# Kernel tuning notes

Measured on AMD Instinct MI355X. Metric: run time of the kernel, lower is better.

## Reference

```python
import jax, jax.numpy as jnp
import numpy as np

N = 40000       # nodes
E = 512000      # edges (avg degree 16)
D = 128         # embed_dim
H = 128         # hidden_dim
R = 8           # num_relations
B = 8           # num_bases
C = 3           # output classes (hardcoded in conv7)


def _prelu(x, a):
    # torch.nn.PReLU(num_parameters=C): per-channel slope
    return jnp.where(x >= 0, x, a * x)


def _rgcn(x, src, dst, etype, bases, comp, root, bias):
    """PyG RGCNConv with basis decomposition, aggr='mean' (default).
    out[i] = sum_r mean_{e: dst=i, type=r} (W_r @ x[src_e]) + root @ x[i] + bias
    W_r = sum_b comp[r,b] * bases[b]. Aggregation is linear, so we aggregate
    source features per (node, relation) first, then apply W_r once per node.
    """
    n = x.shape[0]
    seg = dst * R + etype                      # composite (node, relation) id
    gx = x[src]                                # [E, in]  (big gather)
    agg = jax.ops.segment_sum(gx, seg, num_segments=n * R)              # [N*R, in]
    cnt = jax.ops.segment_sum(jnp.ones((src.shape[0],), x.dtype), seg,
                              num_segments=n * R)                        # [N*R]
    agg = agg / jnp.maximum(cnt, 1.0)[:, None]                           # mean per (node, rel)
    agg = agg.reshape(n, R, -1)                                          # [N, R, in]
    Wr = jnp.einsum('rb,bio->rio', comp, bases)                          # [R, in, out]
    return jnp.einsum('nri,rio->no', agg, Wr) + x @ root + bias


def setup_inputs() -> dict:
    key = jax.random.key(0)
    ks = jax.random.split(key, 20)
    num_x = jax.random.normal(ks[0], (N, 1), jnp.float32)
    x = jax.random.normal(ks[1], (N, D), jnp.float32)
    edge_index = jax.random.randint(ks[2], (2, E), 0, N, jnp.int32)
    edge_type = jax.random.randint(ks[3], (E,), 0, R, jnp.int32)
    # params
    lin_w = jax.random.normal(ks[4], (1, D), jnp.float32) * 0.1
    lin_b = jax.random.normal(ks[5], (D,), jnp.float32) * 0.1
    prelu_a = 0.25 + 0.01 * jax.random.normal(ks[6], (7, D), jnp.float32)
    s = 1.0 / np.sqrt(H)
    bases = jax.random.normal(ks[7], (6, B, H, H), jnp.float32) * s   # conv1..conv6 (in==out==H)
    comp = jax.random.normal(ks[8], (6, R, B), jnp.float32) * (1.0 / np.sqrt(B))
    root = jax.random.normal(ks[9], (6, H, H), jnp.float32) * s
    bias = jax.random.normal(ks[10], (6, H), jnp.float32) * 0.1
    bases7 = jax.random.normal(ks[11], (B, H, C), jnp.float32) * s
    comp7 = jax.random.normal(ks[12], (R, B), jnp.float32) * (1.0 / np.sqrt(B))
    root7 = jax.random.normal(ks[13], (H, C), jnp.float32) * s
    bias7 = jax.random.normal(ks[14], (C,), jnp.float32) * 0.1
    return dict(num_x=num_x, x=x, edge_index=edge_index, edge_type=edge_type,
                lin_w=lin_w, lin_b=lin_b, prelu_a=prelu_a,
                bases=bases, comp=comp, root=root, bias=bias,
                bases7=bases7, comp7=comp7, root7=root7, bias7=bias7)


def reference(num_x, x, edge_index, edge_type, lin_w, lin_b, prelu_a,
              bases, comp, root, bias, bases7, comp7, root7, bias7):
    src, dst = edge_index[0], edge_index[1]
    h = _prelu(num_x @ lin_w + lin_b, prelu_a[0])   # act_lin(num_lin(num_x))
    h = h + x
    for i in range(6):  # conv1..conv6 + PReLU (dropout is identity in eval)
        h = _rgcn(h, src, dst, edge_type, bases[i], comp[i], root[i], bias[i])
        h = _prelu(h, prelu_a[i + 1])
    h = _rgcn(h, src, dst, edge_type, bases7, comp7, root7, bias7)  # conv7 -> 3 classes
    return jax.nn.log_softmax(h, axis=1)
```

## Files before the change

kernel.cpp:

```cpp
#include <hip/hip_runtime.h>

typedef unsigned short ushortT;
typedef ushortT ushort8 __attribute__((ext_vector_type(8)));
typedef short bf16x8 __attribute__((ext_vector_type(8)));
typedef float f32x4 __attribute__((ext_vector_type(4)));
typedef unsigned int uint32;

#define NN 40000
#define NE 512000
#define DD 128
#define RR 8
#define NSEG (NN * RR)
#define KT 1152
#define NB_SCAN 1250

__device__ __forceinline__ float bf2f(ushortT u) { return __uint_as_float(((unsigned)u) << 16); }
__device__ __forceinline__ ushortT f2bf(float f) {
  unsigned u = __float_as_uint(f);
  unsigned r = (u + 0x7fffu + ((u >> 16) & 1u)) >> 16;
  return (ushortT)r;
}

__global__ void count_kernel(const int* __restrict__ dst, const int* __restrict__ et,
                             int* __restrict__ cnt) {
  int e = blockIdx.x * 256 + threadIdx.x;
  if (e < NE) atomicAdd(&cnt[dst[e] * RR + et[e]], 1);
}

__global__ void scan1_kernel(const int* __restrict__ cnt, int* __restrict__ offs,
                             int* __restrict__ bsum) {
  __shared__ int s[256];
  int tid = threadIdx.x, gid = blockIdx.x * 256 + tid;
  int v = cnt[gid];
  s[tid] = v; __syncthreads();
  for (int o = 1; o < 256; o <<= 1) {
    int t = (tid >= o) ? s[tid - o] : 0;
    __syncthreads(); s[tid] += t; __syncthreads();
  }
  offs[gid] = s[tid] - v;
  if (tid == 255) bsum[blockIdx.x] = s[255];
}

__global__ void scan2_kernel(int* __restrict__ bsum) {
  __shared__ int s[256];
  __shared__ int carry, tot;
  int tid = threadIdx.x;
  if (tid == 0) carry = 0;
  __syncthreads();
  for (int base = 0; base < NB_SCAN; base += 256) {
    int i = base + tid;
    int v = (i < NB_SCAN) ? bsum[i] : 0;
    s[tid] = v; __syncthreads();
    for (int o = 1; o < 256; o <<= 1) {
      int t = (tid >= o) ? s[tid - o] : 0;
      __syncthreads(); s[tid] += t; __syncthreads();
    }
    if (i < NB_SCAN) bsum[i] = s[tid] - v + carry;
    if (tid == 255) tot = s[255];
    __syncthreads();
    if (tid == 0) carry += tot;
    __syncthreads();
  }
}

__global__ void scan3_kernel(int* __restrict__ offs, const int* __restrict__ bsum,
                             const int* __restrict__ cnt, int* __restrict__ cursor) {
  int gid = blockIdx.x * 256 + threadIdx.x;
  int v = offs[gid] + bsum[blockIdx.x];
  offs[gid] = v;
  cursor[gid] = v;
  if (gid == NSEG - 1) offs[NSEG] = v + cnt[gid];
}

__global__ void fill_kernel(const int* __restrict__ src, const int* __restrict__ dst,
                            const int* __restrict__ et, int* __restrict__ cursor,
                            int* __restrict__ srcs) {
  int e = blockIdx.x * 256 + threadIdx.x;
  if (e >= NE) return;
  int seg = dst[e] * RR + et[e];
  int slot = atomicAdd(&cursor[seg], 1);
  srcs[slot] = src[e];
}

__global__ void init_h_kernel(const float* __restrict__ num_x, const float* __restrict__ x,
                              const float* __restrict__ lin_w, const float* __restrict__ lin_b,
                              const float* __restrict__ a0, ushortT* __restrict__ h) {
  int idx = blockIdx.x * 256 + threadIdx.x;
  if (idx >= NN * DD) return;
  int n = idx >> 7, d = idx & 127;
  float v = fmaf(num_x[n], lin_w[d], lin_b[d]);
  v = v >= 0.f ? v : a0[d] * v;
  h[idx] = f2bf(v + x[idx]);
}

__global__ void build_w_kernel(const float* __restrict__ bases, const float* __restrict__ comp,
                               const float* __restrict__ root, ushortT* __restrict__ Wt6) {
  int idx = blockIdx.x * 256 + threadIdx.x;
  if (idx >= 6 * DD * KT) return;
  int layer = idx / (DD * KT);
  int rem = idx - layer * (DD * KT);
  int j = rem / KT, k = rem - j * KT;
  const float* B  = bases + (size_t)layer * 8 * DD * DD;
  const float* C  = comp + layer * RR * 8;
  const float* Rt = root + (size_t)layer * DD * DD;
  float s;
  if (k < RR * DD) {
    int r = k >> 7, i = k & 127;
    s = 0.f;
#pragma unroll
    for (int b = 0; b < 8; ++b) s += C[r * 8 + b] * B[(b * DD + i) * DD + j];
  } else {
    s = Rt[(k - RR * DD) * DD + j];
  }
  Wt6[idx] = f2bf(s);
}

__global__ __launch_bounds__(256)
void agg_kernel(const int* __restrict__ offs, const int* __restrict__ srcs,
                const ushortT* __restrict__ h, ushortT* __restrict__ Xagg) {
  int seg = blockIdx.x * 32 + (threadIdx.x >> 3);
  int l = threadIdx.x & 7;
  int beg = offs[seg], end = offs[seg + 1];
  float a[16];
#pragma unroll
  for (int j = 0; j < 16; ++j) a[j] = 0.f;
  int e = beg;
  for (; e + 2 <= end; e += 2) {
    int s0 = srcs[e], s1 = srcs[e + 1];
    const ushortT* p0 = &h[(size_t)s0 * DD + l * 16];
    const ushortT* p1 = &h[(size_t)s1 * DD + l * 16];
    ushort8 v00 = *(const ushort8*)p0;
    ushort8 v01 = *(const ushort8*)(p0 + 8);
    ushort8 v10 = *(const ushort8*)p1;
    ushort8 v11 = *(const ushort8*)(p1 + 8);
#pragma unroll
    for (int j = 0; j < 8; ++j) {
      a[j]     += bf2f(v00[j]) + bf2f(v10[j]);
      a[8 + j] += bf2f(v01[j]) + bf2f(v11[j]);
    }
  }
  if (e < end) {
    int s0 = srcs[e];
    const ushortT* p0 = &h[(size_t)s0 * DD + l * 16];
    ushort8 v00 = *(const ushort8*)p0;
    ushort8 v01 = *(const ushort8*)(p0 + 8);
#pragma unroll
    for (int j = 0; j < 8; ++j) {
      a[j]     += bf2f(v00[j]);
      a[8 + j] += bf2f(v01[j]);
    }
  }
  float inv = (end > beg) ? 1.0f / (float)(end - beg) : 1.0f;
  ushort8 r0, r1;
#pragma unroll
  for (int j = 0; j < 8; ++j) {
    r0[j] = f2bf(a[j] * inv);
    r1[j] = f2bf(a[8 + j] * inv);
  }
  ushortT* op = &Xagg[(size_t)seg * DD + l * 16];
  *(ushort8*)op = r0;
  *(ushort8*)(op + 8) = r1;
}

__global__ __launch_bounds__(256)
void gemm_kernel(const ushortT* __restrict__ Xagg, const ushortT* __restrict__ h,
                 const ushortT* __restrict__ Wt, const float* __restrict__ bias,
                 const float* __restrict__ slope, ushortT* __restrict__ hout) {
  __shared__ ushortT As[64 * 64];
  __shared__ ushortT Bs[128 * 64];
  int tid = threadIdx.x, lane = tid & 63, wv = tid >> 6;
  int wr = wv >> 1, wc = wv & 1;
  int n0 = blockIdx.x * 64;
  int l8 = lane >> 3;
  int lp = lane & 7;
  f32x4 acc[2][4];
#pragma unroll
  for (int m = 0; m < 2; ++m)
#pragma unroll
    for (int n = 0; n < 4; ++n) acc[m][n] = (f32x4){0.f, 0.f, 0.f, 0.f};

  for (int kc = 0; kc < KT; kc += 64) {
#pragma unroll
    for (int j = 0; j < 2; ++j) {
      int row = wv * 16 + j * 8 + l8;
      int p = lp ^ (row & 7);
      const ushortT* g;
      if (kc < RR * DD) g = Xagg + (size_t)(n0 + row) * 1024 + kc + p * 8;
      else              g = h + (size_t)(n0 + row) * DD + (kc - RR * DD) + p * 8;
      __builtin_amdgcn_global_load_lds(
          (const __attribute__((address_space(1))) void*)g,
          (__attribute__((address_space(3))) void*)&As[(wv * 16 + j * 8) * 64], 16, 0, 0);
    }
#pragma unroll
    for (int j = 0; j < 4; ++j) {
      int col = wv * 32 + j * 8 + l8;
      int p = lp ^ (col & 7);
      const ushortT* g = Wt + (size_t)col * KT + kc + p * 8;
      __builtin_amdgcn_global_load_lds(
          (const __attribute__((address_space(1))) void*)g,
          (__attribute__((address_space(3))) void*)&Bs[(wv * 32 + j * 8) * 64], 16, 0, 0);
    }
    __syncthreads();
#pragma unroll
    for (int kk = 0; kk < 2; ++kk) {
      int ko2 = kk * 64 + (lane >> 4) * 16;
      bf16x8 a[2], b[4];
#pragma unroll
      for (int m = 0; m < 2; ++m) {
        int row = wr * 32 + m * 16 + (lane & 15);
        int off = ((row << 7) + ko2) ^ ((row & 7) << 4);
        a[m] = *(const bf16x8*)((const char*)As + off);
      }
#pragma unroll
      for (int n = 0; n < 4; ++n) {
        int col = wc * 64 + n * 16 + (lane & 15);
        int off = ((col << 7) + ko2) ^ ((col & 7) << 4);
        b[n] = *(const bf16x8*)((const char*)Bs + off);
      }
#pragma unroll
      for (int m = 0; m < 2; ++m)
#pragma unroll
        for (int n = 0; n < 4; ++n)
          acc[m][n] = __builtin_amdgcn_mfma_f32_16x16x32_bf16(a[m], b[n], acc[m][n], 0, 0, 0);
    }
    __syncthreads();
  }
#pragma unroll
  for (int m = 0; m < 2; ++m) {
    int row = n0 + wr * 32 + m * 16 + (lane >> 4) * 4;
#pragma unroll
    for (int n = 0; n < 4; ++n) {
      int col = wc * 64 + n * 16 + (lane & 15);
      float bcol = bias[col], scol = slope[col];
#pragma unroll
      for (int q = 0; q < 4; ++q) {
        float v = acc[m][n][q] + bcol;
        v = v >= 0.f ? v : scol * v;
        hout[(size_t)(row + q) * DD + col] = f2bf(v);
      }
    }
  }
}

__global__ void build_w7_kernel(const float* __restrict__ bases7, const float* __restrict__ comp7,
                                const float* __restrict__ root7, float* __restrict__ W7) {
  int idx = blockIdx.x * 256 + threadIdx.x;
  if (idx >= KT * 3) return;
  int row = idx / 3, c = idx - row * 3;
  if (row < RR * DD) {
    int r = row >> 7, i = row & 127;
    float s = 0.f;
#pragma unroll
    for (int b = 0; b < 8; ++b) s += comp7[r * 8 + b] * bases7[(b * DD + i) * 3 + c];
    W7[idx] = s;
  } else {
    W7[idx] = root7[(row - RR * DD) * 3 + c];
  }
}

__global__ void conv7_kernel(const ushortT* __restrict__ Xagg, const ushortT* __restrict__ h,
                             const float* __restrict__ W7, const float* __restrict__ bias7,
                             float* __restrict__ out) {
  int gw = (blockIdx.x * 256 + threadIdx.x) >> 6;
  if (gw >= NN) return;
  int lane = threadIdx.x & 63;
  float a0 = 0.f, a1 = 0.f, a2 = 0.f;
#pragma unroll
  for (int i = 0; i < 2; ++i) {
    int k0 = i * 512 + lane * 8;
    ushort8 v = *(const ushort8*)&Xagg[(size_t)gw * 1024 + k0];
#pragma unroll
    for (int j = 0; j < 8; ++j) {
      float xx = bf2f(v[j]);
      const float* w = &W7[(k0 + j) * 3];
      a0 = fmaf(xx, w[0], a0); a1 = fmaf(xx, w[1], a1); a2 = fmaf(xx, w[2], a2);
    }
  }
  {
    uint32 v = *(const uint32*)&h[(size_t)gw * DD + lane * 2];
    float x0 = __uint_as_float(v << 16), x1 = __uint_as_float(v & 0xffff0000u);
    int k0 = 1024 + lane * 2;
    const float* w0 = &W7[k0 * 3];
    const float* w1 = &W7[(k0 + 1) * 3];
    a0 = fmaf(x0, w0[0], a0); a1 = fmaf(x0, w0[1], a1); a2 = fmaf(x0, w0[2], a2);
    a0 = fmaf(x1, w1[0], a0); a1 = fmaf(x1, w1[1], a1); a2 = fmaf(x1, w1[2], a2);
  }
#pragma unroll
  for (int o = 32; o > 0; o >>= 1) {
    a0 += __shfl_down(a0, o);
    a1 += __shfl_down(a1, o);
    a2 += __shfl_down(a2, o);
  }
  if (lane == 0) {
    float l0 = a0 + bias7[0], l1 = a1 + bias7[1], l2 = a2 + bias7[2];
    float m = fmaxf(l0, fmaxf(l1, l2));
    float lse = m + logf(expf(l0 - m) + expf(l1 - m) + expf(l2 - m));
    out[gw * 3 + 0] = l0 - lse;
    out[gw * 3 + 1] = l1 - lse;
    out[gw * 3 + 2] = l2 - lse;
  }
}

extern "C" void kernel_launch(void* const* d_in, const int* in_sizes, int n_in,
                              void* d_out, int out_size, void* d_ws, size_t ws_size,
                              hipStream_t stream) {
  const float* num_x  = (const float*)d_in[0];
  const float* x      = (const float*)d_in[1];
  const int*   eidx   = (const int*)d_in[2];
  const int*   etype  = (const int*)d_in[3];
  const float* lin_w  = (const float*)d_in[4];
  const float* lin_b  = (const float*)d_in[5];
  const float* prelu  = (const float*)d_in[6];
  const float* bases  = (const float*)d_in[7];
  const float* comp   = (const float*)d_in[8];
  const float* root   = (const float*)d_in[9];
  const float* bias   = (const float*)d_in[10];
  const float* bases7 = (const float*)d_in[11];
  const float* comp7  = (const float*)d_in[12];
  const float* root7  = (const float*)d_in[13];
  const float* bias7  = (const float*)d_in[14];
  const int* srcv = eidx;
  const int* dstv = eidx + NE;
  float* out = (float*)d_out;

  char* p = (char*)d_ws;
  auto alloc = [&](size_t bytes) { char* q = p; p += (bytes + 255) & ~(size_t)255; return q; };
  int*     counts = (int*)alloc((size_t)NSEG * 4);
  int*     offs   = (int*)alloc((size_t)(NSEG + 1) * 4);
  int*     cursor = (int*)alloc((size_t)NSEG * 4);
  int*     bsum   = (int*)alloc((size_t)NB_SCAN * 4);
  int*     srcs   = (int*)alloc((size_t)NE * 4);
  ushortT* h0     = (ushortT*)alloc((size_t)NN * DD * 2);
  ushortT* h1     = (ushortT*)alloc((size_t)NN * DD * 2);
  ushortT* Xagg   = (ushortT*)alloc((size_t)NN * 1024 * 2);
  ushortT* Wt6    = (ushortT*)alloc((size_t)6 * DD * KT * 2);
  float*   W7     = (float*)alloc((size_t)KT * 3 * 4);
  if (ws_size < (size_t)(p - (char*)d_ws)) return;

  hipMemsetAsync(counts, 0, (size_t)NSEG * 4, stream);
  count_kernel<<<NE / 256, 256, 0, stream>>>(dstv, etype, counts);
  scan1_kernel<<<NB_SCAN, 256, 0, stream>>>(counts, offs, bsum);
  scan2_kernel<<<1, 256, 0, stream>>>(bsum);
  scan3_kernel<<<NB_SCAN, 256, 0, stream>>>(offs, bsum, counts, cursor);
  fill_kernel<<<NE / 256, 256, 0, stream>>>(srcv, dstv, etype, cursor, srcs);

  init_h_kernel<<<(NN * DD + 255) / 256, 256, 0, stream>>>(num_x, x, lin_w, lin_b, prelu, h0);
  build_w_kernel<<<(6 * DD * KT + 255) / 256, 256, 0, stream>>>(bases, comp, root, Wt6);
  build_w7_kernel<<<(KT * 3 + 255) / 256, 256, 0, stream>>>(bases7, comp7, root7, W7);

  ushortT* hin = h0;
  ushortT* hout = h1;
  for (int layer = 0; layer < 6; ++layer) {
    agg_kernel<<<NSEG / 32, 256, 0, stream>>>(offs, srcs, hin, Xagg);
    gemm_kernel<<<NN / 64, 256, 0, stream>>>(Xagg, hin, Wt6 + (size_t)layer * DD * KT,
                                             bias + layer * DD, prelu + (layer + 1) * DD, hout);
    ushortT* t = hin; hin = hout; hout = t;
  }
  agg_kernel<<<NSEG / 32, 256, 0, stream>>>(offs, srcs, hin, Xagg);
  conv7_kernel<<<NN / 4, 256, 0, stream>>>(Xagg, hin, W7, bias7, out);
}
```

Before: 474.9 us.

## Double-buffer GEMM LDS tiles and fuse conv7 projection into aggregation

The GEMM now keeps two LDS buffers and issues the next k-tile's global-to-LDS loads before computing the current one, so load latency can overlap the MFMA work. The final layer no longer writes the 80MB bf16 Xagg tensor and reads it back. Each (node, relation) segment is projected straight to the 3 output classes and accumulated with float atomics, and a small final kernel adds the root term and applies log_softmax. Costs are a larger LDS footprint per block, an extra memset, and atomic contention on 8 segments per node, whose float sums are not in a fixed order.

```diff
diff --git a/kernel.cpp b/kernel.cpp
--- a/kernel.cpp
+++ b/kernel.cpp
@@ -166,8 +166,8 @@
 void gemm_kernel(const ushortT* __restrict__ Xagg, const ushortT* __restrict__ h,
                  const ushortT* __restrict__ Wt, const float* __restrict__ bias,
                  const float* __restrict__ slope, ushortT* __restrict__ hout) {
-  __shared__ ushortT As[64 * 64];
-  __shared__ ushortT Bs[128 * 64];
+  __shared__ ushortT As[2][64 * 64];
+  __shared__ ushortT Bs[2][128 * 64];
   int tid = threadIdx.x, lane = tid & 63, wv = tid >> 6;
   int wr = wv >> 1, wc = wv & 1;
   int n0 = blockIdx.x * 64;
@@ -179,7 +179,8 @@
 #pragma unroll
     for (int n = 0; n < 4; ++n) acc[m][n] = (f32x4){0.f, 0.f, 0.f, 0.f};
 
-  for (int kc = 0; kc < KT; kc += 64) {
+  auto stage = [&](int buf, int t) {
+    int kc = t * 64;
 #pragma unroll
     for (int j = 0; j < 2; ++j) {
       int row = wv * 16 + j * 8 + l8;
@@ -189,7 +190,7 @@
       else              g = h + (size_t)(n0 + row) * DD + (kc - RR * DD) + p * 8;
       __builtin_amdgcn_global_load_lds(
           (const __attribute__((address_space(1))) void*)g,
-          (__attribute__((address_space(3))) void*)&As[(wv * 16 + j * 8) * 64], 16, 0, 0);
+          (__attribute__((address_space(3))) void*)&As[buf][(wv * 16 + j * 8) * 64], 16, 0, 0);
     }
 #pragma unroll
     for (int j = 0; j < 4; ++j) {
@@ -198,9 +199,15 @@
       const ushortT* g = Wt + (size_t)col * KT + kc + p * 8;
       __builtin_amdgcn_global_load_lds(
           (const __attribute__((address_space(1))) void*)g,
-          (__attribute__((address_space(3))) void*)&Bs[(wv * 32 + j * 8) * 64], 16, 0, 0);
-    }
-    __syncthreads();
+          (__attribute__((address_space(3))) void*)&Bs[buf][(wv * 32 + j * 8) * 64], 16, 0, 0);
+    }
+  };
+
+  stage(0, 0);
+  __syncthreads();
+  for (int t = 0; t < 18; ++t) {
+    int cur = t & 1;
+    if (t + 1 < 18) stage(cur ^ 1, t + 1);
 #pragma unroll
     for (int kk = 0; kk < 2; ++kk) {
       int ko2 = kk * 64 + (lane >> 4) * 16;
@@ -209,13 +216,13 @@
       for (int m = 0; m < 2; ++m) {
         int row = wr * 32 + m * 16 + (lane & 15);
         int off = ((row << 7) + ko2) ^ ((row & 7) << 4);
-        a[m] = *(const bf16x8*)((const char*)As + off);
+        a[m] = *(const bf16x8*)((const char*)As[cur] + off);
       }
 #pragma unroll
       for (int n = 0; n < 4; ++n) {
         int col = wc * 64 + n * 16 + (lane & 15);
         int off = ((col << 7) + ko2) ^ ((col & 7) << 4);
-        b[n] = *(const bf16x8*)((const char*)Bs + off);
+        b[n] = *(const bf16x8*)((const char*)Bs[cur] + off);
       }
 #pragma unroll
       for (int m = 0; m < 2; ++m)
@@ -258,33 +265,81 @@
   }
 }
 
-__global__ void conv7_kernel(const ushortT* __restrict__ Xagg, const ushortT* __restrict__ h,
-                             const float* __restrict__ W7, const float* __restrict__ bias7,
-                             float* __restrict__ out) {
+__global__ __launch_bounds__(256)
+void agg7c_kernel(const int* __restrict__ offs, const int* __restrict__ srcs,
+                  const ushortT* __restrict__ h, const float* __restrict__ W7,
+                  float* __restrict__ outacc) {
+  int seg = blockIdx.x * 32 + (threadIdx.x >> 3);
+  int l = threadIdx.x & 7;
+  int beg = offs[seg], end = offs[seg + 1];
+  if (end <= beg) return;
+  float a[16];
+#pragma unroll
+  for (int j = 0; j < 16; ++j) a[j] = 0.f;
+  int e = beg;
+  for (; e + 2 <= end; e += 2) {
+    int s0 = srcs[e], s1 = srcs[e + 1];
+    const ushortT* p0 = &h[(size_t)s0 * DD + l * 16];
+    const ushortT* p1 = &h[(size_t)s1 * DD + l * 16];
+    ushort8 v00 = *(const ushort8*)p0;
+    ushort8 v01 = *(const ushort8*)(p0 + 8);
+    ushort8 v10 = *(const ushort8*)p1;
+    ushort8 v11 = *(const ushort8*)(p1 + 8);
+#pragma unroll
+    for (int j = 0; j < 8; ++j) {
+      a[j]     += bf2f(v00[j]) + bf2f(v10[j]);
+      a[8 + j] += bf2f(v01[j]) + bf2f(v11[j]);
+    }
+  }
+  if (e < end) {
+    int s0 = srcs[e];
+    const ushortT* p0 = &h[(size_t)s0 * DD + l * 16];
+    ushort8 v00 = *(const ushort8*)p0;
+    ushort8 v01 = *(const ushort8*)(p0 + 8);
+#pragma unroll
+    for (int j = 0; j < 8; ++j) {
+      a[j]     += bf2f(v00[j]);
+      a[8 + j] += bf2f(v01[j]);
+    }
+  }
+  float inv = 1.0f / (float)(end - beg);
+  int r = seg & 7;
+  const float* w = &W7[((size_t)r * DD + l * 16) * 3];
+  float p0 = 0.f, p1 = 0.f, p2 = 0.f;
+#pragma unroll
+  for (int j = 0; j < 16; ++j) {
+    float x = a[j] * inv;
+    p0 = fmaf(x, w[j * 3 + 0], p0);
+    p1 = fmaf(x, w[j * 3 + 1], p1);
+    p2 = fmaf(x, w[j * 3 + 2], p2);
+  }
+#pragma unroll
+  for (int o = 1; o < 8; o <<= 1) {
+    p0 += __shfl_xor(p0, o);
+    p1 += __shfl_xor(p1, o);
+    p2 += __shfl_xor(p2, o);
+  }
+  if (l == 0) {
+    int node = seg >> 3;
+    atomicAdd(&outacc[node * 3 + 0], p0);
+    atomicAdd(&outacc[node * 3 + 1], p1);
+    atomicAdd(&outacc[node * 3 + 2], p2);
+  }
+}
+
+__global__ __launch_bounds__(256)
+void final_kernel(const float* __restrict__ outacc, const ushortT* __restrict__ h,
+                  const float* __restrict__ W7, const float* __restrict__ bias7,
+                  float* __restrict__ out) {
   int gw = (blockIdx.x * 256 + threadIdx.x) >> 6;
   if (gw >= NN) return;
   int lane = threadIdx.x & 63;
-  float a0 = 0.f, a1 = 0.f, a2 = 0.f;
-#pragma unroll
-  for (int i = 0; i < 2; ++i) {
-    int k0 = i * 512 + lane * 8;
-    ushort8 v = *(const ushort8*)&Xagg[(size_t)gw * 1024 + k0];
-#pragma unroll
-    for (int j = 0; j < 8; ++j) {
-      float xx = bf2f(v[j]);
-      const float* w = &W7[(k0 + j) * 3];
-      a0 = fmaf(xx, w[0], a0); a1 = fmaf(xx, w[1], a1); a2 = fmaf(xx, w[2], a2);
-    }
-  }
-  {
-    uint32 v = *(const uint32*)&h[(size_t)gw * DD + lane * 2];
-    float x0 = __uint_as_float(v << 16), x1 = __uint_as_float(v & 0xffff0000u);
-    int k0 = 1024 + lane * 2;
-    const float* w0 = &W7[k0 * 3];
-    const float* w1 = &W7[(k0 + 1) * 3];
-    a0 = fmaf(x0, w0[0], a0); a1 = fmaf(x0, w0[1], a1); a2 = fmaf(x0, w0[2], a2);
-    a0 = fmaf(x1, w1[0], a0); a1 = fmaf(x1, w1[1], a1); a2 = fmaf(x1, w1[2], a2);
-  }
+  uint32 v = *(const uint32*)&h[(size_t)gw * DD + lane * 2];
+  float x0 = __uint_as_float(v << 16), x1 = __uint_as_float(v & 0xffff0000u);
+  int k0 = (1024 + lane * 2) * 3;
+  float a0 = x0 * W7[k0 + 0] + x1 * W7[k0 + 3];
+  float a1 = x0 * W7[k0 + 1] + x1 * W7[k0 + 4];
+  float a2 = x0 * W7[k0 + 2] + x1 * W7[k0 + 5];
 #pragma unroll
   for (int o = 32; o > 0; o >>= 1) {
     a0 += __shfl_down(a0, o);
@@ -292,7 +347,9 @@
     a2 += __shfl_down(a2, o);
   }
   if (lane == 0) {
-    float l0 = a0 + bias7[0], l1 = a1 + bias7[1], l2 = a2 + bias7[2];
+    float l0 = a0 + outacc[gw * 3 + 0] + bias7[0];
+    float l1 = a1 + outacc[gw * 3 + 1] + bias7[1];
+    float l2 = a2 + outacc[gw * 3 + 2] + bias7[2];
     float m = fmaxf(l0, fmaxf(l1, l2));
     float lse = m + logf(expf(l0 - m) + expf(l1 - m) + expf(l2 - m));
     out[gw * 3 + 0] = l0 - lse;
@@ -335,9 +392,11 @@
   ushortT* Xagg   = (ushortT*)alloc((size_t)NN * 1024 * 2);
   ushortT* Wt6    = (ushortT*)alloc((size_t)6 * DD * KT * 2);
   float*   W7     = (float*)alloc((size_t)KT * 3 * 4);
+  float*   outacc = (float*)alloc((size_t)NN * 3 * 4);
   if (ws_size < (size_t)(p - (char*)d_ws)) return;
 
   hipMemsetAsync(counts, 0, (size_t)NSEG * 4, stream);
+  hipMemsetAsync(outacc, 0, (size_t)NN * 3 * 4, stream);
   count_kernel<<<NE / 256, 256, 0, stream>>>(dstv, etype, counts);
   scan1_kernel<<<NB_SCAN, 256, 0, stream>>>(counts, offs, bsum);
   scan2_kernel<<<1, 256, 0, stream>>>(bsum);
@@ -356,6 +415,6 @@
                                              bias + layer * DD, prelu + (layer + 1) * DD, hout);
     ushortT* t = hin; hin = hout; hout = t;
   }
-  agg_kernel<<<NSEG / 32, 256, 0, stream>>>(offs, srcs, hin, Xagg);
-  conv7_kernel<<<NN / 4, 256, 0, stream>>>(Xagg, hin, W7, bias7, out);
-}
+  agg7c_kernel<<<NSEG / 32, 256, 0, stream>>>(offs, srcs, hin, W7, outacc);
+  final_kernel<<<NN / 4, 256, 0, stream>>>(outacc, hin, W7, bias7, out);
+}
```

Result: slower. 495.3 us (+4.3%).

## Double-buffer GEMM LDS tiles and unroll edge gather by four

Applied to the files above, without the earlier changes.

The GEMM kernel now uses two LDS buffers for A and B. It issues the global-to-LDS loads for the next K chunk before running the MFMAs on the current chunk, so memory latency overlaps with compute. The aggregation kernel now processes four source edges per iteration, which keeps more gather loads in flight, and finishes the remainder with a scalar loop. In exchange, LDS use per block doubles, which may lower occupancy, and the agg kernel needs more registers.

```diff
diff --git a/kernel.cpp b/kernel.cpp
--- a/kernel.cpp
+++ b/kernel.cpp
@@ -125,25 +125,26 @@
 #pragma unroll
   for (int j = 0; j < 16; ++j) a[j] = 0.f;
   int e = beg;
-  for (; e + 2 <= end; e += 2) {
-    int s0 = srcs[e], s1 = srcs[e + 1];
+  for (; e + 4 <= end; e += 4) {
+    int s0 = srcs[e], s1 = srcs[e + 1], s2 = srcs[e + 2], s3 = srcs[e + 3];
     const ushortT* p0 = &h[(size_t)s0 * DD + l * 16];
     const ushortT* p1 = &h[(size_t)s1 * DD + l * 16];
-    ushort8 v00 = *(const ushort8*)p0;
-    ushort8 v01 = *(const ushort8*)(p0 + 8);
-    ushort8 v10 = *(const ushort8*)p1;
-    ushort8 v11 = *(const ushort8*)(p1 + 8);
+    const ushortT* p2 = &h[(size_t)s2 * DD + l * 16];
+    const ushortT* p3 = &h[(size_t)s3 * DD + l * 16];
+    ushort8 v00 = *(const ushort8*)p0, v01 = *(const ushort8*)(p0 + 8);
+    ushort8 v10 = *(const ushort8*)p1, v11 = *(const ushort8*)(p1 + 8);
+    ushort8 v20 = *(const ushort8*)p2, v21 = *(const ushort8*)(p2 + 8);
+    ushort8 v30 = *(const ushort8*)p3, v31 = *(const ushort8*)(p3 + 8);
 #pragma unroll
     for (int j = 0; j < 8; ++j) {
-      a[j]     += bf2f(v00[j]) + bf2f(v10[j]);
-      a[8 + j] += bf2f(v01[j]) + bf2f(v11[j]);
-    }
-  }
-  if (e < end) {
+      a[j]     += (bf2f(v00[j]) + bf2f(v10[j])) + (bf2f(v20[j]) + bf2f(v30[j]));
+      a[8 + j] += (bf2f(v01[j]) + bf2f(v11[j])) + (bf2f(v21[j]) + bf2f(v31[j]));
+    }
+  }
+  for (; e < end; ++e) {
     int s0 = srcs[e];
     const ushortT* p0 = &h[(size_t)s0 * DD + l * 16];
-    ushort8 v00 = *(const ushort8*)p0;
-    ushort8 v01 = *(const ushort8*)(p0 + 8);
+    ushort8 v00 = *(const ushort8*)p0, v01 = *(const ushort8*)(p0 + 8);
 #pragma unroll
     for (int j = 0; j < 8; ++j) {
       a[j]     += bf2f(v00[j]);
@@ -166,8 +167,8 @@
 void gemm_kernel(const ushortT* __restrict__ Xagg, const ushortT* __restrict__ h,
                  const ushortT* __restrict__ Wt, const float* __restrict__ bias,
                  const float* __restrict__ slope, ushortT* __restrict__ hout) {
-  __shared__ ushortT As[64 * 64];
-  __shared__ ushortT Bs[128 * 64];
+  __shared__ ushortT As[2][64 * 64];
+  __shared__ ushortT Bs[2][128 * 64];
   int tid = threadIdx.x, lane = tid & 63, wv = tid >> 6;
   int wr = wv >> 1, wc = wv & 1;
   int n0 = blockIdx.x * 64;
@@ -179,7 +180,8 @@
 #pragma unroll
     for (int n = 0; n < 4; ++n) acc[m][n] = (f32x4){0.f, 0.f, 0.f, 0.f};
 
-  for (int kc = 0; kc < KT; kc += 64) {
+  auto stage = [&](int buf, int t) {
+    int kc = t * 64;
 #pragma unroll
     for (int j = 0; j < 2; ++j) {
       int row = wv * 16 + j * 8 + l8;
@@ -189,7 +191,7 @@
       else              g = h + (size_t)(n0 + row) * DD + (kc - RR * DD) + p * 8;
       __builtin_amdgcn_global_load_lds(
           (const __attribute__((address_space(1))) void*)g,
-          (__attribute__((address_space(3))) void*)&As[(wv * 16 + j * 8) * 64], 16, 0, 0);
+          (__attribute__((address_space(3))) void*)&As[buf][(wv * 16 + j * 8) * 64], 16, 0, 0);
     }
 #pragma unroll
     for (int j = 0; j < 4; ++j) {
@@ -198,9 +200,15 @@
       const ushortT* g = Wt + (size_t)col * KT + kc + p * 8;
       __builtin_amdgcn_global_load_lds(
           (const __attribute__((address_space(1))) void*)g,
-          (__attribute__((address_space(3))) void*)&Bs[(wv * 32 + j * 8) * 64], 16, 0, 0);
-    }
-    __syncthreads();
+          (__attribute__((address_space(3))) void*)&Bs[buf][(wv * 32 + j * 8) * 64], 16, 0, 0);
+    }
+  };
+
+  stage(0, 0);
+  __syncthreads();
+  for (int t = 0; t < 18; ++t) {
+    int cur = t & 1;
+    if (t + 1 < 18) stage(cur ^ 1, t + 1);
 #pragma unroll
     for (int kk = 0; kk < 2; ++kk) {
       int ko2 = kk * 64 + (lane >> 4) * 16;
@@ -209,13 +217,13 @@
       for (int m = 0; m < 2; ++m) {
         int row = wr * 32 + m * 16 + (lane & 15);
         int off = ((row << 7) + ko2) ^ ((row & 7) << 4);
-        a[m] = *(const bf16x8*)((const char*)As + off);
+        a[m] = *(const bf16x8*)((const char*)As[cur] + off);
       }
 #pragma unroll
       for (int n = 0; n < 4; ++n) {
         int col = wc * 64 + n * 16 + (lane & 15);
         int off = ((col << 7) + ko2) ^ ((col & 7) << 4);
-        b[n] = *(const bf16x8*)((const char*)Bs + off);
+        b[n] = *(const bf16x8*)((const char*)Bs[cur] + off);
       }
 #pragma unroll
       for (int m = 0; m < 2; ++m)
```

Result: slower. 516.7 us (+8.8%).

## Double-buffer GEMM LDS tiles and stage edge source indices in shared memory

Applied to the files above, without the earlier changes.

The GEMM kernel now uses two LDS buffers, so it issues the async global-to-LDS loads for the next K tile while computing MFMAs on the current one, hiding load latency. The aggregation kernel cooperatively loads the block's segment offsets and up to ECAP source indices into shared memory before gathering, with a global fallback beyond the cap. The cost is doubled GEMM LDS usage, which may lower occupancy, and extra barriers in the aggregation kernel.

```diff
diff --git a/kernel.cpp b/kernel.cpp
--- a/kernel.cpp
+++ b/kernel.cpp
@@ -13,6 +13,7 @@
 #define NSEG (NN * RR)
 #define KT 1152
 #define NB_SCAN 1250
+#define ECAP 320
 
 __device__ __forceinline__ float bf2f(ushortT u) { return __uint_as_float(((unsigned)u) << 16); }
 __device__ __forceinline__ ushortT f2bf(float f) {
@@ -118,15 +119,28 @@
 __global__ __launch_bounds__(256)
 void agg_kernel(const int* __restrict__ offs, const int* __restrict__ srcs,
                 const ushortT* __restrict__ h, ushortT* __restrict__ Xagg) {
-  int seg = blockIdx.x * 32 + (threadIdx.x >> 3);
-  int l = threadIdx.x & 7;
-  int beg = offs[seg], end = offs[seg + 1];
+  __shared__ int s_offs[33];
+  __shared__ int s_srcs[ECAP];
+  int tid = threadIdx.x;
+  int sb = blockIdx.x * 32;
+  if (tid < 33) s_offs[tid] = offs[sb + tid];
+  __syncthreads();
+  int e_base = s_offs[0];
+  int nE = s_offs[32] - e_base;
+  for (int i = tid; i < nE && i < ECAP; i += 256) s_srcs[i] = srcs[e_base + i];
+  __syncthreads();
+
+  int g = tid >> 3;
+  int l = tid & 7;
+  int beg = s_offs[g], end = s_offs[g + 1];
   float a[16];
 #pragma unroll
   for (int j = 0; j < 16; ++j) a[j] = 0.f;
   int e = beg;
   for (; e + 2 <= end; e += 2) {
-    int s0 = srcs[e], s1 = srcs[e + 1];
+    int i0 = e - e_base, i1 = i0 + 1;
+    int s0 = (i0 < ECAP) ? s_srcs[i0] : srcs[e];
+    int s1 = (i1 < ECAP) ? s_srcs[i1] : srcs[e + 1];
     const ushortT* p0 = &h[(size_t)s0 * DD + l * 16];
     const ushortT* p1 = &h[(size_t)s1 * DD + l * 16];
     ushort8 v00 = *(const ushort8*)p0;
@@ -140,7 +154,8 @@
     }
   }
   if (e < end) {
-    int s0 = srcs[e];
+    int i0 = e - e_base;
+    int s0 = (i0 < ECAP) ? s_srcs[i0] : srcs[e];
     const ushortT* p0 = &h[(size_t)s0 * DD + l * 16];
     ushort8 v00 = *(const ushort8*)p0;
     ushort8 v01 = *(const ushort8*)(p0 + 8);
@@ -157,7 +172,7 @@
     r0[j] = f2bf(a[j] * inv);
     r1[j] = f2bf(a[8 + j] * inv);
   }
-  ushortT* op = &Xagg[(size_t)seg * DD + l * 16];
+  ushortT* op = &Xagg[(size_t)(sb + g) * DD + l * 16];
   *(ushort8*)op = r0;
   *(ushort8*)(op + 8) = r1;
 }
@@ -166,8 +181,8 @@
 void gemm_kernel(const ushortT* __restrict__ Xagg, const ushortT* __restrict__ h,
                  const ushortT* __restrict__ Wt, const float* __restrict__ bias,
                  const float* __restrict__ slope, ushortT* __restrict__ hout) {
-  __shared__ ushortT As[64 * 64];
-  __shared__ ushortT Bs[128 * 64];
+  __shared__ ushortT As[2][64 * 64];
+  __shared__ ushortT Bs[2][128 * 64];
   int tid = threadIdx.x, lane = tid & 63, wv = tid >> 6;
   int wr = wv >> 1, wc = wv & 1;
   int n0 = blockIdx.x * 64;
@@ -179,7 +194,8 @@
 #pragma unroll
     for (int n = 0; n < 4; ++n) acc[m][n] = (f32x4){0.f, 0.f, 0.f, 0.f};
 
-  for (int kc = 0; kc < KT; kc += 64) {
+  auto stage = [&](int buf, int t) {
+    int kc = t * 64;
 #pragma unroll
     for (int j = 0; j < 2; ++j) {
       int row = wv * 16 + j * 8 + l8;
@@ -189,7 +205,7 @@
       else              g = h + (size_t)(n0 + row) * DD + (kc - RR * DD) + p * 8;
       __builtin_amdgcn_global_load_lds(
           (const __attribute__((address_space(1))) void*)g,
-          (__attribute__((address_space(3))) void*)&As[(wv * 16 + j * 8) * 64], 16, 0, 0);
+          (__attribute__((address_space(3))) void*)&As[buf][(wv * 16 + j * 8) * 64], 16, 0, 0);
     }
 #pragma unroll
     for (int j = 0; j < 4; ++j) {
@@ -198,9 +214,15 @@
       const ushortT* g = Wt + (size_t)col * KT + kc + p * 8;
       __builtin_amdgcn_global_load_lds(
           (const __attribute__((address_space(1))) void*)g,
-          (__attribute__((address_space(3))) void*)&Bs[(wv * 32 + j * 8) * 64], 16, 0, 0);
-    }
-    __syncthreads();
+          (__attribute__((address_space(3))) void*)&Bs[buf][(wv * 32 + j * 8) * 64], 16, 0, 0);
+    }
+  };
+
+  stage(0, 0);
+  __syncthreads();
+  for (int t = 0; t < 18; ++t) {
+    int cur = t & 1;
+    if (t + 1 < 18) stage(cur ^ 1, t + 1);
 #pragma unroll
     for (int kk = 0; kk < 2; ++kk) {
       int ko2 = kk * 64 + (lane >> 4) * 16;
@@ -209,13 +231,13 @@
       for (int m = 0; m < 2; ++m) {
         int row = wr * 32 + m * 16 + (lane & 15);
         int off = ((row << 7) + ko2) ^ ((row & 7) << 4);
-        a[m] = *(const bf16x8*)((const char*)As + off);
+        a[m] = *(const bf16x8*)((const char*)As[cur] + off);
       }
 #pragma unroll
       for (int n = 0; n < 4; ++n) {
         int col = wc * 64 + n * 16 + (lane & 15);
         int off = ((col << 7) + ko2) ^ ((col & 7) << 4);
-        b[n] = *(const bf16x8*)((const char*)Bs + off);
+        b[n] = *(const bf16x8*)((const char*)Bs[cur] + off);
       }
 #pragma unroll
       for (int m = 0; m < 2; ++m)
```

New measurement: 469.9 us, median of 2. Within noise of the previous version (-1.1%).
